# Kernel tuning notes

Hardware: AMD Instinct MI355X
Metric: run time of the kernel (lower is better)

Reference implementation:

```python
import jax, jax.numpy as jnp
import numpy as np

_EPS = 1e-6


def setup_inputs() -> dict:
    key = jax.random.key(0)
    k1, k2, k3, k4 = jax.random.split(key, 4)
    B, N = 32, 131072
    xyz_s = jax.random.normal(k1, (B, 3, N), dtype=jnp.float32)
    weighted_t = jax.random.normal(k2, (B, 3, N), dtype=jnp.float32)
    weights = jax.random.uniform(k3, (B, 1, N), dtype=jnp.float32)
    label = jax.random.randint(k4, (B, 1, N), 0, 2).astype(jnp.float32)
    return {"xyz_s": xyz_s, "weighted_t": weighted_t, "weights": weights, "label": label}


def reference(xyz_s, weighted_t, weights, label):
    # background mask: |label - 1|
    background = jnp.abs(label - 1.0)            # (B,1,N)
    w = (weights * background)[:, 0, :]          # (B,N)
    xs = jnp.swapaxes(xyz_s, 1, 2)               # (B,N,3) source points
    xt = jnp.swapaxes(weighted_t, 1, 2)          # (B,N,3) target points

    # normalized weights
    wn = w[..., None] / (jnp.sum(w, axis=1, keepdims=True)[..., None] + _EPS)  # (B,N,1)

    # weighted centroids
    centroid_s = jnp.sum(xs * wn, axis=1)        # (B,3)
    centroid_t = jnp.sum(xt * wn, axis=1)        # (B,3)

    s_centered = xs - centroid_s[:, None, :]
    t_centered = xt - centroid_t[:, None, :]

    # weighted covariance: s_centered^T @ (t_centered * wn) -> (B,3,3)
    cov = jnp.einsum('bnd,bne->bde', s_centered, t_centered * wn)

    u, s, vh = jnp.linalg.svd(cov)               # cov = u @ diag(s) @ vh
    v = jnp.swapaxes(vh, -1, -2)
    ut = jnp.swapaxes(u, -1, -2)

    rot_pos = v @ ut
    v_neg = v.at[:, :, 2].multiply(-1.0)         # flip last column of V
    rot_neg = v_neg @ ut
    det_pos = jnp.linalg.det(rot_pos)
    rot = jnp.where(det_pos[:, None, None] > 0, rot_pos, rot_neg)  # (B,3,3)

    translation = -rot @ centroid_s[..., None] + centroid_t[..., None]  # (B,3,1)
    return rot, translation
```

## Files before the change

### kernel.cpp

```cpp
#include <hip/hip_runtime.h>
#include <math.h>

#define N_PTS 131072
#define BPB   64
#define CHUNK (N_PTS / BPB)
#define TPB   256
#define NACC  16
#define NITER (CHUNK / 4 / TPB)

__global__ __launch_bounds__(TPB) void ego_partial_kernel(
    const float* __restrict__ xyz_s,
    const float* __restrict__ wtgt,
    const float* __restrict__ weights,
    const float* __restrict__ label,
    float* __restrict__ partials)
{
    const int b     = blockIdx.y;
    const int chunk = blockIdx.x;
    const int t     = threadIdx.x;

    const size_t baseN  = (size_t)b * N_PTS + (size_t)chunk * CHUNK;
    const size_t base3  = (size_t)b * 3 * N_PTS + (size_t)chunk * CHUNK;

    const float4* w4  = (const float4*)(weights + baseN);
    const float4* l4  = (const float4*)(label   + baseN);
    const float4* xs0 = (const float4*)(xyz_s + base3);
    const float4* xs1 = (const float4*)(xyz_s + base3 + N_PTS);
    const float4* xs2 = (const float4*)(xyz_s + base3 + 2 * N_PTS);
    const float4* xt0 = (const float4*)(wtgt  + base3);
    const float4* xt1 = (const float4*)(wtgt  + base3 + N_PTS);
    const float4* xt2 = (const float4*)(wtgt  + base3 + 2 * N_PTS);

    float4 wv[NITER], lv[NITER];
    float4 a0[NITER], a1[NITER], a2[NITER];
    float4 b0[NITER], b1[NITER], b2[NITER];
#pragma unroll
    for (int k = 0; k < NITER; ++k) {
        const int i = t + k * TPB;
        wv[k] = w4[i];
        lv[k] = l4[i];
        a0[k] = xs0[i]; a1[k] = xs1[i]; a2[k] = xs2[i];
        b0[k] = xt0[i]; b1[k] = xt1[i]; b2[k] = xt2[i];
    }

    float acc[NACC];
#pragma unroll
    for (int i = 0; i < NACC; ++i) acc[i] = 0.0f;

#pragma unroll
    for (int k = 0; k < NITER; ++k) {
#define ACCUM(C)                                              \
        {                                                     \
            const float w  = wv[k].C * fabsf(lv[k].C - 1.0f); \
            const float s0 = a0[k].C, s1 = a1[k].C, s2 = a2[k].C; \
            const float t0 = b0[k].C, t1 = b1[k].C, t2 = b2[k].C; \
            acc[0] += w;                                      \
            const float ws0 = w * s0, ws1 = w * s1, ws2 = w * s2; \
            acc[1] += ws0;  acc[2] += ws1;  acc[3] += ws2;    \
            acc[4] += w * t0; acc[5] += w * t1; acc[6] += w * t2; \
            acc[7]  += ws0 * t0; acc[8]  += ws0 * t1; acc[9]  += ws0 * t2; \
            acc[10] += ws1 * t0; acc[11] += ws1 * t1; acc[12] += ws1 * t2; \
            acc[13] += ws2 * t0; acc[14] += ws2 * t1; acc[15] += ws2 * t2; \
        }
        ACCUM(x) ACCUM(y) ACCUM(z) ACCUM(w)
#undef ACCUM
    }

#pragma unroll
    for (int i = 0; i < NACC; ++i) {
        float v = acc[i];
#pragma unroll
        for (int off = 32; off > 0; off >>= 1)
            v += __shfl_down(v, off, 64);
        acc[i] = v;
    }

    __shared__ float red[TPB / 64][NACC];
    const int wave = t >> 6;
    const int lane = t & 63;
    if (lane == 0) {
#pragma unroll
        for (int i = 0; i < NACC; ++i) red[wave][i] = acc[i];
    }
    __syncthreads();

    if (t < NACC) {
        float v = 0.0f;
#pragma unroll
        for (int wv_ = 0; wv_ < TPB / 64; ++wv_) v += red[wv_][t];
        partials[((size_t)b * BPB + chunk) * NACC + t] = v;
    }
}

__global__ __launch_bounds__(64) void ego_finalize_kernel(
    const float* __restrict__ partials,
    float* __restrict__ out,
    int B)
{
    const int b = blockIdx.x;
    const int t = threadIdx.x;

    double acc[NACC];
    const float* p = partials + ((size_t)b * BPB + t) * NACC;
#pragma unroll
    for (int i = 0; i < NACC; ++i) acc[i] = (double)p[i];

#pragma unroll
    for (int i = 0; i < NACC; ++i) {
        double v = acc[i];
#pragma unroll
        for (int off = 32; off > 0; off >>= 1)
            v += __shfl_down(v, off, 64);
        acc[i] = v;
    }

    if (t != 0) return;

    const double W     = acc[0];
    const double denom = W + 1e-6;
    double cs[3], ct[3];
#pragma unroll
    for (int d = 0; d < 3; ++d) {
        cs[d] = acc[1 + d] / denom;
        ct[d] = acc[4 + d] / denom;
    }
    const double Wn = W / denom;

    double cov[3][3];
#pragma unroll
    for (int d = 0; d < 3; ++d)
#pragma unroll
        for (int e = 0; e < 3; ++e)
            cov[d][e] = acc[7 + d * 3 + e] / denom - cs[d] * ct[e] * (2.0 - Wn);

    double Bm[3][3];
    for (int i = 0; i < 3; ++i)
        for (int j = 0; j < 3; ++j) {
            double s = 0.0;
            for (int k = 0; k < 3; ++k) s += cov[k][i] * cov[k][j];
            Bm[i][j] = s;
        }
    double V[3][3] = {{1,0,0},{0,1,0},{0,0,1}};

    for (int sweep = 0; sweep < 8; ++sweep) {
        const int pq[3][2] = {{0,1},{0,2},{1,2}};
        for (int r = 0; r < 3; ++r) {
            const int pp = pq[r][0], qq = pq[r][1];
            const double apq = Bm[pp][qq];
            if (fabs(apq) < 1e-300) continue;
            const double tau = (Bm[qq][qq] - Bm[pp][pp]) / (2.0 * apq);
            const double tt  = (tau >= 0.0 ? 1.0 : -1.0) /
                               (fabs(tau) + sqrt(1.0 + tau * tau));
            const double c = 1.0 / sqrt(1.0 + tt * tt);
            const double s = tt * c;
            for (int k = 0; k < 3; ++k) {
                const double bkp = Bm[k][pp], bkq = Bm[k][qq];
                Bm[k][pp] = c * bkp - s * bkq;
                Bm[k][qq] = s * bkp + c * bkq;
            }
            for (int k = 0; k < 3; ++k) {
                const double bpk = Bm[pp][k], bqk = Bm[qq][k];
                Bm[pp][k] = c * bpk - s * bqk;
                Bm[qq][k] = s * bpk + c * bqk;
            }
            for (int k = 0; k < 3; ++k) {
                const double vkp = V[k][pp], vkq = V[k][qq];
                V[k][pp] = c * vkp - s * vkq;
                V[k][qq] = s * vkp + c * vkq;
            }
        }
    }

    double lam[3] = {Bm[0][0], Bm[1][1], Bm[2][2]};
    int idx[3] = {0, 1, 2};
    for (int i = 0; i < 2; ++i)
        for (int j = i + 1; j < 3; ++j)
            if (lam[idx[j]] > lam[idx[i]]) { int tmp = idx[i]; idx[i] = idx[j]; idx[j] = tmp; }
    double Vs[3][3];
    for (int c = 0; c < 3; ++c)
        for (int rr = 0; rr < 3; ++rr) Vs[rr][c] = V[rr][idx[c]];

    double U[3][3];
    for (int c = 0; c < 3; ++c) {
        double u0 = 0, u1 = 0, u2 = 0;
        for (int k = 0; k < 3; ++k) {
            u0 += cov[0][k] * Vs[k][c];
            u1 += cov[1][k] * Vs[k][c];
            u2 += cov[2][k] * Vs[k][c];
        }
        const double nn = sqrt(u0 * u0 + u1 * u1 + u2 * u2);
        if (nn > 1e-150) {
            U[0][c] = u0 / nn; U[1][c] = u1 / nn; U[2][c] = u2 / nn;
        } else if (c == 2) {
            U[0][2] = U[1][0] * U[2][1] - U[2][0] * U[1][1];
            U[1][2] = U[2][0] * U[0][1] - U[0][0] * U[2][1];
            U[2][2] = U[0][0] * U[1][1] - U[1][0] * U[0][1];
        } else {
            U[0][c] = (c == 0); U[1][c] = (c == 1); U[2][c] = 0.0;
        }
    }

    double rot[3][3];
    for (int d = 0; d < 3; ++d)
        for (int e = 0; e < 3; ++e)
            rot[d][e] = Vs[d][0] * U[e][0] + Vs[d][1] * U[e][1] + Vs[d][2] * U[e][2];

    const double det =
        rot[0][0] * (rot[1][1] * rot[2][2] - rot[1][2] * rot[2][1]) -
        rot[0][1] * (rot[1][0] * rot[2][2] - rot[1][2] * rot[2][0]) +
        rot[0][2] * (rot[1][0] * rot[2][1] - rot[1][1] * rot[2][0]);

    if (!(det > 0.0)) {
        for (int d = 0; d < 3; ++d)
            for (int e = 0; e < 3; ++e)
                rot[d][e] = Vs[d][0] * U[e][0] + Vs[d][1] * U[e][1] - Vs[d][2] * U[e][2];
    }

    double tr[3];
    for (int d = 0; d < 3; ++d)
        tr[d] = -(rot[d][0] * cs[0] + rot[d][1] * cs[1] + rot[d][2] * cs[2]) + ct[d];

    for (int d = 0; d < 3; ++d)
        for (int e = 0; e < 3; ++e)
            out[(size_t)b * 9 + d * 3 + e] = (float)rot[d][e];
    for (int d = 0; d < 3; ++d)
        out[(size_t)B * 9 + (size_t)b * 3 + d] = (float)tr[d];
}

extern "C" void kernel_launch(void* const* d_in, const int* in_sizes, int n_in,
                              void* d_out, int out_size, void* d_ws, size_t ws_size,
                              hipStream_t stream) {
    const float* xyz_s   = (const float*)d_in[0];
    const float* wtgt    = (const float*)d_in[1];
    const float* weights = (const float*)d_in[2];
    const float* label   = (const float*)d_in[3];
    float* out = (float*)d_out;
    float* partials = (float*)d_ws;

    const int B = in_sizes[2] / N_PTS;

    dim3 grid1(BPB, B);
    ego_partial_kernel<<<grid1, TPB, 0, stream>>>(xyz_s, wtgt, weights, label, partials);
    ego_finalize_kernel<<<B, 64, 0, stream>>>(partials, out, B);
}
```

Baseline: 163.3 us.

## Fuse reduction and SVD solve via atomic last-block pattern with double-buffered loads

Merges the partial-sum and finalize kernels into one launch: each block atomically adds its 16 sums into per-batch float accumulators, and the last block (found with an atomic counter) runs the 3x3 SVD solve. It also halves the blocks per batch and swaps the load-everything-then-compute loop for a two-buffer load/consume pipeline, lowering register pressure. This removes a kernel launch and the partials round trip, but adds a memset launch and float atomics. The final sums are now accumulated in float rather than double, with non-deterministic ordering.

```diff
diff --git a/kernel.cpp b/kernel.cpp
--- a/kernel.cpp
+++ b/kernel.cpp
@@ -2,18 +2,25 @@
 #include <math.h>
 
 #define N_PTS 131072
-#define BPB   64
+#define BPB   32
 #define CHUNK (N_PTS / BPB)
 #define TPB   256
 #define NACC  16
 #define NITER (CHUNK / 4 / TPB)
 
-__global__ __launch_bounds__(TPB) void ego_partial_kernel(
+#define WS_SUMS_FLOATS (32 * NACC)
+#define WS_BYTES (WS_SUMS_FLOATS * 4 + 32 * 4)
+
+__device__ void ego_solve(const double* acc, float* out, int b, int B);
+
+__global__ __launch_bounds__(TPB) void ego_fused_kernel(
     const float* __restrict__ xyz_s,
     const float* __restrict__ wtgt,
     const float* __restrict__ weights,
     const float* __restrict__ label,
-    float* __restrict__ partials)
+    float* __restrict__ sums,
+    int*   __restrict__ counters,
+    float* __restrict__ out, int B)
 {
     const int b     = blockIdx.y;
     const int chunk = blockIdx.x;
@@ -31,29 +38,24 @@
     const float4* xt1 = (const float4*)(wtgt  + base3 + N_PTS);
     const float4* xt2 = (const float4*)(wtgt  + base3 + 2 * N_PTS);
 
-    float4 wv[NITER], lv[NITER];
-    float4 a0[NITER], a1[NITER], a2[NITER];
-    float4 b0[NITER], b1[NITER], b2[NITER];
-#pragma unroll
-    for (int k = 0; k < NITER; ++k) {
-        const int i = t + k * TPB;
-        wv[k] = w4[i];
-        lv[k] = l4[i];
-        a0[k] = xs0[i]; a1[k] = xs1[i]; a2[k] = xs2[i];
-        b0[k] = xt0[i]; b1[k] = xt1[i]; b2[k] = xt2[i];
-    }
-
     float acc[NACC];
 #pragma unroll
     for (int i = 0; i < NACC; ++i) acc[i] = 0.0f;
 
-#pragma unroll
-    for (int k = 0; k < NITER; ++k) {
-#define ACCUM(C)                                              \
+    float4 wvA, lvA, a0A, a1A, a2A, b0A, b1A, b2A;
+    float4 wvB, lvB, a0B, a1B, a2B, b0B, b1B, b2B;
+
+#define LOADBUF(S, k)                                    \
+    {   const int i_ = t + (k) * TPB;                    \
+        wv##S = w4[i_];  lv##S = l4[i_];                 \
+        a0##S = xs0[i_]; a1##S = xs1[i_]; a2##S = xs2[i_]; \
+        b0##S = xt0[i_]; b1##S = xt1[i_]; b2##S = xt2[i_]; }
+
+#define ACCUM1(S, C)                                          \
         {                                                     \
-            const float w  = wv[k].C * fabsf(lv[k].C - 1.0f); \
-            const float s0 = a0[k].C, s1 = a1[k].C, s2 = a2[k].C; \
-            const float t0 = b0[k].C, t1 = b1[k].C, t2 = b2[k].C; \
+            const float w  = wv##S.C * fabsf(lv##S.C - 1.0f); \
+            const float s0 = a0##S.C, s1 = a1##S.C, s2 = a2##S.C; \
+            const float t0 = b0##S.C, t1 = b1##S.C, t2 = b2##S.C; \
             acc[0] += w;                                      \
             const float ws0 = w * s0, ws1 = w * s1, ws2 = w * s2; \
             acc[1] += ws0;  acc[2] += ws1;  acc[3] += ws2;    \
@@ -62,9 +64,20 @@
             acc[10] += ws1 * t0; acc[11] += ws1 * t1; acc[12] += ws1 * t2; \
             acc[13] += ws2 * t0; acc[14] += ws2 * t1; acc[15] += ws2 * t2; \
         }
-        ACCUM(x) ACCUM(y) ACCUM(z) ACCUM(w)
-#undef ACCUM
-    }
+#define CONSUME(S) ACCUM1(S, x) ACCUM1(S, y) ACCUM1(S, z) ACCUM1(S, w)
+
+    LOADBUF(A, 0)
+    LOADBUF(B, 1)
+    CONSUME(A)
+    LOADBUF(A, 2)
+    CONSUME(B)
+    LOADBUF(B, 3)
+    CONSUME(A)
+    CONSUME(B)
+
+#undef LOADBUF
+#undef ACCUM1
+#undef CONSUME
 
 #pragma unroll
     for (int i = 0; i < NACC; ++i) {
@@ -88,34 +101,31 @@
         float v = 0.0f;
 #pragma unroll
         for (int wv_ = 0; wv_ < TPB / 64; ++wv_) v += red[wv_][t];
-        partials[((size_t)b * BPB + chunk) * NACC + t] = v;
+        atomicAdd(&sums[b * NACC + t], v);
+    }
+
+    __shared__ int is_last;
+    if (t == 0) {
+        __threadfence();
+        const int old = atomicAdd(&counters[b], 1);
+        is_last = (old == BPB - 1) ? 1 : 0;
+    }
+    __syncthreads();
+
+    if (is_last && t == 0) {
+        __threadfence();
+        double acc_d[NACC];
+#pragma unroll
+        for (int i = 0; i < NACC; ++i)
+            acc_d[i] = (double)__hip_atomic_load(&sums[b * NACC + i],
+                                                 __ATOMIC_ACQUIRE,
+                                                 __HIP_MEMORY_SCOPE_AGENT);
+        ego_solve(acc_d, out, b, B);
     }
 }
 
-__global__ __launch_bounds__(64) void ego_finalize_kernel(
-    const float* __restrict__ partials,
-    float* __restrict__ out,
-    int B)
+__device__ void ego_solve(const double* acc, float* out, int b, int B)
 {
-    const int b = blockIdx.x;
-    const int t = threadIdx.x;
-
-    double acc[NACC];
-    const float* p = partials + ((size_t)b * BPB + t) * NACC;
-#pragma unroll
-    for (int i = 0; i < NACC; ++i) acc[i] = (double)p[i];
-
-#pragma unroll
-    for (int i = 0; i < NACC; ++i) {
-        double v = acc[i];
-#pragma unroll
-        for (int off = 32; off > 0; off >>= 1)
-            v += __shfl_down(v, off, 64);
-        acc[i] = v;
-    }
-
-    if (t != 0) return;
-
     const double W     = acc[0];
     const double denom = W + 1e-6;
     double cs[3], ct[3];
@@ -235,11 +245,15 @@
     const float* weights = (const float*)d_in[2];
     const float* label   = (const float*)d_in[3];
     float* out = (float*)d_out;
-    float* partials = (float*)d_ws;
+
+    float* sums     = (float*)d_ws;
+    int*   counters = (int*)((char*)d_ws + WS_SUMS_FLOATS * 4);
 
     const int B = in_sizes[2] / N_PTS;
 
-    dim3 grid1(BPB, B);
-    ego_partial_kernel<<<grid1, TPB, 0, stream>>>(xyz_s, wtgt, weights, label, partials);
-    ego_finalize_kernel<<<B, 64, 0, stream>>>(partials, out, B);
+    hipMemsetAsync(d_ws, 0, WS_BYTES, stream);
+
+    dim3 grid(BPB, B);
+    ego_fused_kernel<<<grid, TPB, 0, stream>>>(xyz_s, wtgt, weights, label,
+                                               sums, counters, out, B);
 }
```

Result: slower. 234.7 us (+43.7%).
